# Kernel tuning notes

Hardware: AMD Instinct MI355X
Metric: run time of the kernel (lower is better)

Reference implementation:

```python
import jax, jax.numpy as jnp
import numpy as np

N_NODES = 200000  # num_users + num_items
N_EDGES = 1000000
D = 64


def setup_inputs() -> dict:
    key = jax.random.key(0)
    ks = jax.random.split(key, 9)
    return {
        "src": jax.random.randint(ks[0], (N_EDGES,), 0, N_NODES, dtype=jnp.int32),
        "dst": jax.random.randint(ks[1], (N_EDGES,), 0, N_NODES, dtype=jnp.int32),
        "review_feat": jax.random.normal(ks[2], (N_EDGES, D), dtype=jnp.float32),
        "ci_r": jax.random.uniform(ks[3], (N_NODES, 1), dtype=jnp.float32),
        "feature": jax.random.normal(ks[4], (N_NODES, D), dtype=jnp.float32),
        "W1": jax.random.normal(ks[5], (D, D), dtype=jnp.float32) * 0.05,
        "W2": jax.random.normal(ks[6], (D, D), dtype=jnp.float32) * 0.05,
        "feature2": jax.random.normal(ks[7], (N_NODES, D), dtype=jnp.float32) * 0.05,
        "feature3": jax.random.normal(ks[8], (N_NODES, D), dtype=jnp.float32) * 0.05,
    }


def reference(src, dst, review_feat, ci_r, feature, W1, W2, feature2, feature3):
    # Eval-mode forward (is_training=False, freeze='', dropout = identity).
    # `feature` is assigned to g.srcdata['h_r'] in the original but never used.
    n = ci_r.shape[0]
    ci_src = ci_r[src]            # [E,1] gather of src norm coeff
    ci_dst = ci_r                 # [N,1]

    # Pass 1: edge linear on review features, scaled by src coeff, scatter-sum.
    r = review_feat @ W1.T                                   # [E,64]
    h1 = jax.ops.segment_sum(r * ci_src, dst, num_segments=n)
    rst_re = h1 * ci_dst

    # Pass 2: (src embedding + edge transform) messages.
    r_fe = review_feat @ W2.T                                # [E,64]
    m2 = (feature2[src] + r_fe) * ci_src
    h2 = jax.ops.segment_sum(m2, dst, num_segments=n)
    rst = h2 * ci_dst

    # Pass 3: pure src-embedding messages.
    m3 = feature3[src] * ci_src
    h3 = jax.ops.segment_sum(m3, dst, num_segments=n)
    rst_id = h3 * ci_dst

    return (rst, rst_re, rst_id)
```

## Files before the change

### kernel.cpp

```cpp
#include <hip/hip_runtime.h>

#define NN 200000
#define NE 1000000
#define DD 64
#define NCHUNK 196

typedef __bf16 bf16x4 __attribute__((ext_vector_type(4)));
typedef __bf16 bf16x8 __attribute__((ext_vector_type(8)));
typedef float  f32x4  __attribute__((ext_vector_type(4)));

static __device__ __forceinline__ bf16x8 pack8(const float* __restrict__ p) {
    float4 a = *reinterpret_cast<const float4*>(p);
    float4 b = *reinterpret_cast<const float4*>(p + 4);
    bf16x8 r;
    r[0] = (__bf16)a.x; r[1] = (__bf16)a.y; r[2] = (__bf16)a.z; r[3] = (__bf16)a.w;
    r[4] = (__bf16)b.x; r[5] = (__bf16)b.y; r[6] = (__bf16)b.z; r[7] = (__bf16)b.w;
    return r;
}

__global__ __launch_bounds__(256) void k_zero(int* __restrict__ counts) {
    const int i = (blockIdx.x * 256 + threadIdx.x) * 4;
    if (i + 3 < NN) {
        *reinterpret_cast<int4*>(counts + i) = make_int4(0, 0, 0, 0);
    } else {
        for (int j = i; j < NN; ++j) counts[j] = 0;
    }
}

__global__ __launch_bounds__(256) void k_hist(const int* __restrict__ dst,
                                              int* __restrict__ counts) {
    for (int e = blockIdx.x * blockDim.x + threadIdx.x; e < NE;
         e += gridDim.x * blockDim.x)
        atomicAdd(&counts[dst[e]], 1);
}

__global__ __launch_bounds__(256) void k_chunk_sums(const int* __restrict__ counts,
                                                    int* __restrict__ csum) {
    const int b = blockIdx.x, tid = threadIdx.x;
    const int base = b * 1024 + tid * 4;
    int s = 0;
#pragma unroll
    for (int j = 0; j < 4; ++j) {
        const int i = base + j;
        if (i < NN) s += counts[i];
    }
#pragma unroll
    for (int d = 32; d > 0; d >>= 1) s += __shfl_down(s, d);
    __shared__ int wsum[4];
    if ((tid & 63) == 0) wsum[tid >> 6] = s;
    __syncthreads();
    if (tid == 0) csum[b] = wsum[0] + wsum[1] + wsum[2] + wsum[3];
}

__global__ void k_scan_chunks(const int* __restrict__ csum, int* __restrict__ cofs) {
    if (threadIdx.x == 0 && blockIdx.x == 0) {
        int acc = 0;
        for (int i = 0; i < NCHUNK; ++i) { cofs[i] = acc; acc += csum[i]; }
    }
}

__global__ __launch_bounds__(256) void k_chunk_scan(const int* __restrict__ counts,
                                                    const int* __restrict__ cofs,
                                                    int* __restrict__ offs,
                                                    int* __restrict__ cursor) {
    const int b = blockIdx.x, tid = threadIdx.x;
    const int lane = tid & 63, wv = tid >> 6;
    const int base = b * 1024 + tid * 4;
    int c[4];
#pragma unroll
    for (int j = 0; j < 4; ++j) {
        const int i = base + j;
        c[j] = (i < NN) ? counts[i] : 0;
    }
    const int ls = c[0] + c[1] + c[2] + c[3];
    int v = ls;
#pragma unroll
    for (int d = 1; d < 64; d <<= 1) {
        const int u = __shfl_up(v, d);
        if (lane >= d) v += u;
    }
    __shared__ int wsum[4];
    if (lane == 63) wsum[wv] = v;
    __syncthreads();
    int wbase = 0;
    for (int w = 0; w < wv; ++w) wbase += wsum[w];
    int excl = cofs[b] + wbase + (v - ls);
#pragma unroll
    for (int j = 0; j < 4; ++j) {
        const int i = base + j;
        if (i < NN) { offs[i] = excl; cursor[i] = excl; }
        excl += c[j];
    }
}

__global__ __launch_bounds__(256) void k_permfill_msg(
    const int* __restrict__ dst, const int* __restrict__ src,
    const float* __restrict__ ci, const float* __restrict__ review,
    int* __restrict__ cursor, __bf16* __restrict__ mrev, int2* __restrict__ esrc)
{
    const int tid = threadIdx.x;
    const int l16 = tid & 15;
    const int e   = blockIdx.x * 16 + (tid >> 4);

    const int s = src[e];
    const float cs = ci[s];
    int pos = 0;
    if (l16 == 0) pos = atomicAdd(&cursor[dst[e]], 1);
    pos = __shfl(pos, tid & 48);

    const float4 r = *reinterpret_cast<const float4*>(review + (size_t)e * DD + l16 * 4);
    bf16x4 m;
    m[0] = (__bf16)(r.x * cs); m[1] = (__bf16)(r.y * cs);
    m[2] = (__bf16)(r.z * cs); m[3] = (__bf16)(r.w * cs);
    *reinterpret_cast<bf16x4*>(mrev + (size_t)pos * DD + l16 * 4) = m;
    if (l16 == 0) esrc[pos] = make_int2(s, __float_as_int(cs));
}

__global__ __launch_bounds__(256) void k_pull_fused(
    const __bf16* __restrict__ mrev, const int2* __restrict__ esrc,
    const int* __restrict__ offs, const int* __restrict__ counts,
    const float* __restrict__ ci,
    const float* __restrict__ f2, const float* __restrict__ f3,
    const float* __restrict__ W1, const float* __restrict__ W2,
    float* __restrict__ out_rst, float* __restrict__ out_re,
    float* __restrict__ out_id)
{
    __shared__ __bf16 At[16][64];
    __shared__ float  S2[16][64];

    const int tid = threadIdx.x;
    const int l16 = tid & 15;
    const int q   = tid >> 4;
    const int n   = blockIdx.x * 16 + q;

    const int beg = offs[n];
    const int cnt = counts[n];

    float4 ax0 = {0,0,0,0}, a20 = {0,0,0,0}, a30 = {0,0,0,0};
    float4 ax1 = {0,0,0,0}, a21 = {0,0,0,0}, a31 = {0,0,0,0};

    int k = 0;
    for (; k + 2 <= cnt; k += 2) {
        const int2 ea = esrc[beg + k];
        const int2 eb = esrc[beg + k + 1];
        const float ca = __int_as_float(ea.y);
        const float cb = __int_as_float(eb.y);
        const bf16x4 ma = *reinterpret_cast<const bf16x4*>(mrev + (size_t)(beg + k) * DD + l16 * 4);
        const bf16x4 mb = *reinterpret_cast<const bf16x4*>(mrev + (size_t)(beg + k + 1) * DD + l16 * 4);
        const float4 p2a = *reinterpret_cast<const float4*>(f2 + (size_t)ea.x * DD + l16 * 4);
        const float4 p2b = *reinterpret_cast<const float4*>(f2 + (size_t)eb.x * DD + l16 * 4);
        const float4 p3a = *reinterpret_cast<const float4*>(f3 + (size_t)ea.x * DD + l16 * 4);
        const float4 p3b = *reinterpret_cast<const float4*>(f3 + (size_t)eb.x * DD + l16 * 4);
        ax0.x += (float)ma[0]; ax0.y += (float)ma[1];
        ax0.z += (float)ma[2]; ax0.w += (float)ma[3];
        ax1.x += (float)mb[0]; ax1.y += (float)mb[1];
        ax1.z += (float)mb[2]; ax1.w += (float)mb[3];
        a20.x = fmaf(p2a.x, ca, a20.x); a20.y = fmaf(p2a.y, ca, a20.y);
        a20.z = fmaf(p2a.z, ca, a20.z); a20.w = fmaf(p2a.w, ca, a20.w);
        a21.x = fmaf(p2b.x, cb, a21.x); a21.y = fmaf(p2b.y, cb, a21.y);
        a21.z = fmaf(p2b.z, cb, a21.z); a21.w = fmaf(p2b.w, cb, a21.w);
        a30.x = fmaf(p3a.x, ca, a30.x); a30.y = fmaf(p3a.y, ca, a30.y);
        a30.z = fmaf(p3a.z, ca, a30.z); a30.w = fmaf(p3a.w, ca, a30.w);
        a31.x = fmaf(p3b.x, cb, a31.x); a31.y = fmaf(p3b.y, cb, a31.y);
        a31.z = fmaf(p3b.z, cb, a31.z); a31.w = fmaf(p3b.w, cb, a31.w);
    }
    if (k < cnt) {
        const int2 ea = esrc[beg + k];
        const float ca = __int_as_float(ea.y);
        const bf16x4 ma = *reinterpret_cast<const bf16x4*>(mrev + (size_t)(beg + k) * DD + l16 * 4);
        const float4 p2a = *reinterpret_cast<const float4*>(f2 + (size_t)ea.x * DD + l16 * 4);
        const float4 p3a = *reinterpret_cast<const float4*>(f3 + (size_t)ea.x * DD + l16 * 4);
        ax0.x += (float)ma[0]; ax0.y += (float)ma[1];
        ax0.z += (float)ma[2]; ax0.w += (float)ma[3];
        a20.x = fmaf(p2a.x, ca, a20.x); a20.y = fmaf(p2a.y, ca, a20.y);
        a20.z = fmaf(p2a.z, ca, a20.z); a20.w = fmaf(p2a.w, ca, a20.w);
        a30.x = fmaf(p3a.x, ca, a30.x); a30.y = fmaf(p3a.y, ca, a30.y);
        a30.z = fmaf(p3a.z, ca, a30.z); a30.w = fmaf(p3a.w, ca, a30.w);
    }

    const float cid = ci[n];
    float4 ax = {ax0.x + ax1.x, ax0.y + ax1.y, ax0.z + ax1.z, ax0.w + ax1.w};
    float4 a2 = {a20.x + a21.x, a20.y + a21.y, a20.z + a21.z, a20.w + a21.w};
    float4 a3 = {a30.x + a31.x, a30.y + a31.y, a30.z + a31.z, a30.w + a31.w};

    float4 v3 = {a3.x * cid, a3.y * cid, a3.z * cid, a3.w * cid};
    *reinterpret_cast<float4*>(out_id + (size_t)n * DD + l16 * 4) = v3;

    bf16x4 hb;
    hb[0] = (__bf16)(ax.x * cid); hb[1] = (__bf16)(ax.y * cid);
    hb[2] = (__bf16)(ax.z * cid); hb[3] = (__bf16)(ax.w * cid);
    *reinterpret_cast<bf16x4*>(&At[q][l16 * 4]) = hb;
    float4 s2v = {a2.x * cid, a2.y * cid, a2.z * cid, a2.w * cid};
    *reinterpret_cast<float4*>(&S2[q][l16 * 4]) = s2v;
    __syncthreads();

    const int w  = tid >> 6;
    const int lq = (tid & 63) >> 4;
    bf16x8 w1f[2], w2f[2];
#pragma unroll
    for (int kk = 0; kk < 2; ++kk) {
        const int off = (w * 16 + l16) * DD + kk * 32 + lq * 8;
        w1f[kk] = pack8(W1 + off);
        w2f[kk] = pack8(W2 + off);
    }
    const bf16x8 a0 = *reinterpret_cast<const bf16x8*>(&At[l16][lq * 8]);
    const bf16x8 a1 = *reinterpret_cast<const bf16x8*>(&At[l16][lq * 8 + 32]);

    const f32x4 zero = {0.f, 0.f, 0.f, 0.f};
    f32x4 acc1 = zero, acc2 = zero;
    acc1 = __builtin_amdgcn_mfma_f32_16x16x32_bf16(a0, w1f[0], acc1, 0, 0, 0);
    acc1 = __builtin_amdgcn_mfma_f32_16x16x32_bf16(a1, w1f[1], acc1, 0, 0, 0);
    acc2 = __builtin_amdgcn_mfma_f32_16x16x32_bf16(a0, w2f[0], acc2, 0, 0, 0);
    acc2 = __builtin_amdgcn_mfma_f32_16x16x32_bf16(a1, w2f[1], acc2, 0, 0, 0);

    const int base = blockIdx.x * 16;
#pragma unroll
    for (int i = 0; i < 4; ++i) {
        const int row = lq * 4 + i;
        const size_t o = (size_t)(base + row) * DD + w * 16 + l16;
        out_re[o]  = acc1[i];
        out_rst[o] = acc2[i] + S2[row][w * 16 + l16];
    }
}

__global__ __launch_bounds__(256) void gcn_mfma_kernel(
    const int* __restrict__ src, const int* __restrict__ dst,
    const float* __restrict__ review, const float* __restrict__ ci,
    const float* __restrict__ W1, const float* __restrict__ W2,
    const float* __restrict__ f2, const float* __restrict__ f3,
    float* __restrict__ out)
{
    float* out_rst = out;
    float* out_re  = out + (size_t)NN * DD;
    float* out_id  = out + 2 * (size_t)NN * DD;
    const int lane = threadIdx.x & 63;
    const int l16  = lane & 15;
    const int lq   = lane >> 4;
    const int wid  = blockIdx.x * (blockDim.x >> 6) + (threadIdx.x >> 6);
    const int nw   = gridDim.x * (blockDim.x >> 6);

    bf16x8 w1f[4][2], w2f[4][2];
#pragma unroll
    for (int c = 0; c < 4; ++c)
#pragma unroll
        for (int kk = 0; kk < 2; ++kk) {
            const int off = (c * 16 + l16) * DD + kk * 32 + lq * 8;
            w1f[c][kk] = pack8(W1 + off);
            w2f[c][kk] = pack8(W2 + off);
        }
    const f32x4 zero = {0.f, 0.f, 0.f, 0.f};
    for (int t = wid; t < NE / 16; t += nw) {
        const int e0 = t * 16;
        const float* xr = review + (size_t)(e0 + l16) * DD + lq * 8;
        const bf16x8 a0 = pack8(xr);
        const bf16x8 a1 = pack8(xr + 32);
        f32x4 acc1[4], acc2[4];
#pragma unroll
        for (int c = 0; c < 4; ++c) { acc1[c] = zero; acc2[c] = zero; }
#pragma unroll
        for (int c = 0; c < 4; ++c) {
            acc1[c] = __builtin_amdgcn_mfma_f32_16x16x32_bf16(a0, w1f[c][0], acc1[c], 0, 0, 0);
            acc1[c] = __builtin_amdgcn_mfma_f32_16x16x32_bf16(a1, w1f[c][1], acc1[c], 0, 0, 0);
            acc2[c] = __builtin_amdgcn_mfma_f32_16x16x32_bf16(a0, w2f[c][0], acc2[c], 0, 0, 0);
            acc2[c] = __builtin_amdgcn_mfma_f32_16x16x32_bf16(a1, w2f[c][1], acc2[c], 0, 0, 0);
        }
        int sA[4], dA[4]; float cf[4];
#pragma unroll
        for (int i = 0; i < 4; ++i) {
            const int e = e0 + lq * 4 + i;
            sA[i] = src[e]; dA[i] = dst[e];
            cf[i] = ci[sA[i]] * ci[dA[i]];
        }
#pragma unroll
        for (int i = 0; i < 4; ++i) {
            const size_t so = (size_t)sA[i] * DD;
            const size_t dofs = (size_t)dA[i] * DD;
            const float c_ = cf[i];
#pragma unroll
            for (int c = 0; c < 4; ++c) {
                const int col = c * 16 + l16;
                atomicAdd(out_re  + dofs + col, acc1[c][i] * c_);
                atomicAdd(out_rst + dofs + col, (f2[so + col] + acc2[c][i]) * c_);
                atomicAdd(out_id  + dofs + col, f3[so + col] * c_);
            }
        }
    }
}

extern "C" void kernel_launch(void* const* d_in, const int* in_sizes, int n_in,
                              void* d_out, int out_size, void* d_ws, size_t ws_size,
                              hipStream_t stream) {
    const int*   src    = (const int*)d_in[0];
    const int*   dst    = (const int*)d_in[1];
    const float* review = (const float*)d_in[2];
    const float* ci     = (const float*)d_in[3];
    const float* W1     = (const float*)d_in[5];
    const float* W2     = (const float*)d_in[6];
    const float* f2     = (const float*)d_in[7];
    const float* f3     = (const float*)d_in[8];
    float* out = (float*)d_out;
    float* out_rst = out;
    float* out_re  = out + (size_t)NN * DD;
    float* out_id  = out + 2 * (size_t)NN * DD;

    const size_t NEED = sizeof(int) * ((size_t)3 * NN + 512) +
                        sizeof(int2) * (size_t)NE +
                        sizeof(__bf16) * (size_t)NE * DD;
    if (ws_size < NEED) {
        hipMemsetAsync(out, 0, (size_t)out_size * sizeof(float), stream);
        gcn_mfma_kernel<<<2048, 256, 0, stream>>>(src, dst, review, ci, W1, W2, f2, f3, out);
        return;
    }

    char* w = (char*)d_ws;
    int* counts = (int*)w;    w += (size_t)NN * 4;
    int* offs   = (int*)w;    w += (size_t)NN * 4;
    int* cursor = (int*)w;    w += (size_t)NN * 4;
    int* csum   = (int*)w;    w += 256 * 4;
    int* cofs   = (int*)w;    w += 256 * 4;
    int2* esrc  = (int2*)w;   w += (size_t)NE * 8;
    __bf16* mrev = (__bf16*)w;

    k_zero        <<<(NN / 4 + 255) / 256, 256, 0, stream>>>(counts);
    k_hist        <<<1024, 256, 0, stream>>>(dst, counts);
    k_chunk_sums  <<<NCHUNK, 256, 0, stream>>>(counts, csum);
    k_scan_chunks <<<1, 64, 0, stream>>>(csum, cofs);
    k_chunk_scan  <<<NCHUNK, 256, 0, stream>>>(counts, cofs, offs, cursor);
    k_permfill_msg<<<NE / 16, 256, 0, stream>>>(dst, src, ci, review, cursor, mrev, esrc);
    k_pull_fused  <<<NN / 16, 256, 0, stream>>>(mrev, esrc, offs, counts, ci,
                                                f2, f3, W1, W2,
                                                out_rst, out_re, out_id);
}
```

Baseline: 316.1 us.

## Gather review rows directly in pull kernel instead of materializing bf16 permuted copy

Result: faster. 295.8 us (-6.4%).

```diff
diff --git a/kernel.cpp b/kernel.cpp
--- a/kernel.cpp
+++ b/kernel.cpp
@@ -20,11 +20,8 @@
 
 __global__ __launch_bounds__(256) void k_zero(int* __restrict__ counts) {
     const int i = (blockIdx.x * 256 + threadIdx.x) * 4;
-    if (i + 3 < NN) {
-        *reinterpret_cast<int4*>(counts + i) = make_int4(0, 0, 0, 0);
-    } else {
-        for (int j = i; j < NN; ++j) counts[j] = 0;
-    }
+    if (i + 3 < NN) *reinterpret_cast<int4*>(counts + i) = make_int4(0, 0, 0, 0);
+    else for (int j = i; j < NN; ++j) counts[j] = 0;
 }
 
 __global__ __launch_bounds__(256) void k_hist(const int* __restrict__ dst,
@@ -93,40 +90,31 @@
     }
 }
 
-__global__ __launch_bounds__(256) void k_permfill_msg(
-    const int* __restrict__ dst, const int* __restrict__ src,
-    const float* __restrict__ ci, const float* __restrict__ review,
-    int* __restrict__ cursor, __bf16* __restrict__ mrev, int2* __restrict__ esrc)
-{
-    const int tid = threadIdx.x;
-    const int l16 = tid & 15;
-    const int e   = blockIdx.x * 16 + (tid >> 4);
-
-    const int s = src[e];
-    const float cs = ci[s];
-    int pos = 0;
-    if (l16 == 0) pos = atomicAdd(&cursor[dst[e]], 1);
-    pos = __shfl(pos, tid & 48);
-
-    const float4 r = *reinterpret_cast<const float4*>(review + (size_t)e * DD + l16 * 4);
-    bf16x4 m;
-    m[0] = (__bf16)(r.x * cs); m[1] = (__bf16)(r.y * cs);
-    m[2] = (__bf16)(r.z * cs); m[3] = (__bf16)(r.w * cs);
-    *reinterpret_cast<bf16x4*>(mrev + (size_t)pos * DD + l16 * 4) = m;
-    if (l16 == 0) esrc[pos] = make_int2(s, __float_as_int(cs));
+__global__ __launch_bounds__(256) void k_permfill(const int* __restrict__ dst,
+                                                  const int* __restrict__ src,
+                                                  const float* __restrict__ ci,
+                                                  int* __restrict__ cursor,
+                                                  int4* __restrict__ epack) {
+    for (int e = blockIdx.x * blockDim.x + threadIdx.x; e < NE;
+         e += gridDim.x * blockDim.x) {
+        const int s = src[e];
+        const float cs = ci[s];
+        const int pos = atomicAdd(&cursor[dst[e]], 1);
+        epack[pos] = make_int4(e, s, __float_as_int(cs), 0);
+    }
 }
 
 __global__ __launch_bounds__(256) void k_pull_fused(
-    const __bf16* __restrict__ mrev, const int2* __restrict__ esrc,
-    const int* __restrict__ offs, const int* __restrict__ counts,
+    const int4* __restrict__ epack, const int* __restrict__ offs,
+    const int* __restrict__ counts, const float* __restrict__ review,
     const float* __restrict__ ci,
     const float* __restrict__ f2, const float* __restrict__ f3,
     const float* __restrict__ W1, const float* __restrict__ W2,
     float* __restrict__ out_rst, float* __restrict__ out_re,
     float* __restrict__ out_id)
 {
-    __shared__ __bf16 At[16][64];
-    __shared__ float  S2[16][64];
+    __shared__ __bf16 At[16][72];
+    __shared__ float  S2[16][68];
 
     const int tid = threadIdx.x;
     const int l16 = tid & 15;
@@ -141,20 +129,20 @@
 
     int k = 0;
     for (; k + 2 <= cnt; k += 2) {
-        const int2 ea = esrc[beg + k];
-        const int2 eb = esrc[beg + k + 1];
-        const float ca = __int_as_float(ea.y);
-        const float cb = __int_as_float(eb.y);
-        const bf16x4 ma = *reinterpret_cast<const bf16x4*>(mrev + (size_t)(beg + k) * DD + l16 * 4);
-        const bf16x4 mb = *reinterpret_cast<const bf16x4*>(mrev + (size_t)(beg + k + 1) * DD + l16 * 4);
-        const float4 p2a = *reinterpret_cast<const float4*>(f2 + (size_t)ea.x * DD + l16 * 4);
-        const float4 p2b = *reinterpret_cast<const float4*>(f2 + (size_t)eb.x * DD + l16 * 4);
-        const float4 p3a = *reinterpret_cast<const float4*>(f3 + (size_t)ea.x * DD + l16 * 4);
-        const float4 p3b = *reinterpret_cast<const float4*>(f3 + (size_t)eb.x * DD + l16 * 4);
-        ax0.x += (float)ma[0]; ax0.y += (float)ma[1];
-        ax0.z += (float)ma[2]; ax0.w += (float)ma[3];
-        ax1.x += (float)mb[0]; ax1.y += (float)mb[1];
-        ax1.z += (float)mb[2]; ax1.w += (float)mb[3];
+        const int4 ea = epack[beg + k];
+        const int4 eb = epack[beg + k + 1];
+        const float ca = __int_as_float(ea.z);
+        const float cb = __int_as_float(eb.z);
+        const float4 ra  = *reinterpret_cast<const float4*>(review + (size_t)ea.x * DD + l16 * 4);
+        const float4 rb  = *reinterpret_cast<const float4*>(review + (size_t)eb.x * DD + l16 * 4);
+        const float4 p2a = *reinterpret_cast<const float4*>(f2 + (size_t)ea.y * DD + l16 * 4);
+        const float4 p2b = *reinterpret_cast<const float4*>(f2 + (size_t)eb.y * DD + l16 * 4);
+        const float4 p3a = *reinterpret_cast<const float4*>(f3 + (size_t)ea.y * DD + l16 * 4);
+        const float4 p3b = *reinterpret_cast<const float4*>(f3 + (size_t)eb.y * DD + l16 * 4);
+        ax0.x = fmaf(ra.x, ca, ax0.x); ax0.y = fmaf(ra.y, ca, ax0.y);
+        ax0.z = fmaf(ra.z, ca, ax0.z); ax0.w = fmaf(ra.w, ca, ax0.w);
+        ax1.x = fmaf(rb.x, cb, ax1.x); ax1.y = fmaf(rb.y, cb, ax1.y);
+        ax1.z = fmaf(rb.z, cb, ax1.z); ax1.w = fmaf(rb.w, cb, ax1.w);
         a20.x = fmaf(p2a.x, ca, a20.x); a20.y = fmaf(p2a.y, ca, a20.y);
         a20.z = fmaf(p2a.z, ca, a20.z); a20.w = fmaf(p2a.w, ca, a20.w);
         a21.x = fmaf(p2b.x, cb, a21.x); a21.y = fmaf(p2b.y, cb, a21.y);
@@ -165,13 +153,13 @@
         a31.z = fmaf(p3b.z, cb, a31.z); a31.w = fmaf(p3b.w, cb, a31.w);
     }
     if (k < cnt) {
-        const int2 ea = esrc[beg + k];
-        const float ca = __int_as_float(ea.y);
-        const bf16x4 ma = *reinterpret_cast<const bf16x4*>(mrev + (size_t)(beg + k) * DD + l16 * 4);
-        const float4 p2a = *reinterpret_cast<const float4*>(f2 + (size_t)ea.x * DD + l16 * 4);
-        const float4 p3a = *reinterpret_cast<const float4*>(f3 + (size_t)ea.x * DD + l16 * 4);
-        ax0.x += (float)ma[0]; ax0.y += (float)ma[1];
-        ax0.z += (float)ma[2]; ax0.w += (float)ma[3];
+        const int4 ea = epack[beg + k];
+        const float ca = __int_as_float(ea.z);
+        const float4 ra  = *reinterpret_cast<const float4*>(review + (size_t)ea.x * DD + l16 * 4);
+        const float4 p2a = *reinterpret_cast<const float4*>(f2 + (size_t)ea.y * DD + l16 * 4);
+        const float4 p3a = *reinterpret_cast<const float4*>(f3 + (size_t)ea.y * DD + l16 * 4);
+        ax0.x = fmaf(ra.x, ca, ax0.x); ax0.y = fmaf(ra.y, ca, ax0.y);
+        ax0.z = fmaf(ra.z, ca, ax0.z); ax0.w = fmaf(ra.w, ca, ax0.w);
         a20.x = fmaf(p2a.x, ca, a20.x); a20.y = fmaf(p2a.y, ca, a20.y);
         a20.z = fmaf(p2a.z, ca, a20.z); a20.w = fmaf(p2a.w, ca, a20.w);
         a30.x = fmaf(p3a.x, ca, a30.x); a30.y = fmaf(p3a.y, ca, a30.y);
@@ -183,8 +171,8 @@
     float4 a2 = {a20.x + a21.x, a20.y + a21.y, a20.z + a21.z, a20.w + a21.w};
     float4 a3 = {a30.x + a31.x, a30.y + a31.y, a30.z + a31.z, a30.w + a31.w};
 
-    float4 v3 = {a3.x * cid, a3.y * cid, a3.z * cid, a3.w * cid};
-    *reinterpret_cast<float4*>(out_id + (size_t)n * DD + l16 * 4) = v3;
+    f32x4 v3 = {a3.x * cid, a3.y * cid, a3.z * cid, a3.w * cid};
+    __builtin_nontemporal_store(v3, reinterpret_cast<f32x4*>(out_id + (size_t)n * DD + l16 * 4));
 
     bf16x4 hb;
     hb[0] = (__bf16)(ax.x * cid); hb[1] = (__bf16)(ax.y * cid);
@@ -218,8 +206,8 @@
     for (int i = 0; i < 4; ++i) {
         const int row = lq * 4 + i;
         const size_t o = (size_t)(base + row) * DD + w * 16 + l16;
-        out_re[o]  = acc1[i];
-        out_rst[o] = acc2[i] + S2[row][w * 16 + l16];
+        __builtin_nontemporal_store(acc1[i], out_re + o);
+        __builtin_nontemporal_store(acc2[i] + S2[row][w * 16 + l16], out_rst + o);
     }
 }
 
@@ -304,10 +292,9 @@
     float* out_id  = out + 2 * (size_t)NN * DD;
 
     const size_t NEED = sizeof(int) * ((size_t)3 * NN + 512) +
-                        sizeof(int2) * (size_t)NE +
-                        sizeof(__bf16) * (size_t)NE * DD;
+                        sizeof(int4) * (size_t)NE;
     if (ws_size < NEED) {
-        hipMemsetAsync(out, 0, (size_t)out_size * sizeof(float), stream);
+        (void)hipMemsetAsync(out, 0, (size_t)out_size * sizeof(float), stream);
         gcn_mfma_kernel<<<2048, 256, 0, stream>>>(src, dst, review, ci, W1, W2, f2, f3, out);
         return;
     }
@@ -318,16 +305,15 @@
     int* cursor = (int*)w;    w += (size_t)NN * 4;
     int* csum   = (int*)w;    w += 256 * 4;
     int* cofs   = (int*)w;    w += 256 * 4;
-    int2* esrc  = (int2*)w;   w += (size_t)NE * 8;
-    __bf16* mrev = (__bf16*)w;
+    int4* epack = (int4*)w;
 
     k_zero        <<<(NN / 4 + 255) / 256, 256, 0, stream>>>(counts);
     k_hist        <<<1024, 256, 0, stream>>>(dst, counts);
     k_chunk_sums  <<<NCHUNK, 256, 0, stream>>>(counts, csum);
     k_scan_chunks <<<1, 64, 0, stream>>>(csum, cofs);
     k_chunk_scan  <<<NCHUNK, 256, 0, stream>>>(counts, cofs, offs, cursor);
-    k_permfill_msg<<<NE / 16, 256, 0, stream>>>(dst, src, ci, review, cursor, mrev, esrc);
-    k_pull_fused  <<<NN / 16, 256, 0, stream>>>(mrev, esrc, offs, counts, ci,
+    k_permfill    <<<1024, 256, 0, stream>>>(dst, src, ci, cursor, epack);
+    k_pull_fused  <<<NN / 16, 256, 0, stream>>>(epack, offs, counts, review, ci,
                                                 f2, f3, W1, W2,
                                                 out_rst, out_re, out_id);
 }
```
